# Optimization experiments

Hardware: AMD Instinct MI355X
Metric: run time of the kernel (lower is better)

Reference implementation:

```python
import jax, jax.numpy as jnp
import numpy as np

N_NODES = 50000
N_EDGES = 800000
N_ENTS = 200000
N_RELS = 500
D = 128


def setup_inputs() -> dict:
    key = jax.random.key(0)
    ks = jax.random.split(key, 9)
    return {
        "prev_ent_embs": jax.random.normal(ks[0], (N_ENTS, D), dtype=jnp.float32),
        "rel_embs": jax.random.normal(ks[1], (N_RELS, D), dtype=jnp.float32),
        "loop_weight": jax.random.normal(ks[2], (D, D), dtype=jnp.float32) * 0.1,
        "evolve_loop_weight": jax.random.normal(ks[3], (D, D), dtype=jnp.float32) * 0.1,
        "weight_neighbor": jax.random.normal(ks[4], (D, D), dtype=jnp.float32) * 0.1,
        "node_id": jax.random.randint(ks[5], (N_NODES,), 0, N_ENTS, dtype=jnp.int64) if jax.config.jax_enable_x64 else jax.random.randint(ks[5], (N_NODES,), 0, N_ENTS, dtype=jnp.int32),
        "src": jax.random.randint(ks[6], (N_EDGES,), 0, N_NODES, dtype=jnp.int32),
        "dst": jax.random.randint(ks[7], (N_EDGES,), 0, N_NODES, dtype=jnp.int32),
        "etype": jax.random.randint(ks[8], (N_EDGES,), 0, N_RELS, dtype=jnp.int32),
    }


def reference(prev_ent_embs, rel_embs, loop_weight, evolve_loop_weight,
              weight_neighbor, node_id, src, dst, etype):
    n_nodes = node_id.shape[0]
    # node features gathered from global entity table
    h = prev_ent_embs[node_id]                                    # [N, D]

    # per-edge message: (h[src] + rel[type]) @ W_neighbor
    msg = (h[src] + rel_embs[etype]) @ weight_neighbor            # [E, D]

    # scatter-sum into destination nodes
    agg = jax.ops.segment_sum(msg, dst, num_segments=n_nodes)     # [N, D]

    # in-degree and norm (apply_func: h * in_norm, standard 1/in_degree)
    deg = jax.ops.segment_sum(jnp.ones_like(dst, dtype=h.dtype), dst,
                              num_segments=n_nodes)               # [N]
    has_in = deg > 0
    in_norm = jnp.where(has_in, 1.0 / jnp.maximum(deg, 1.0), 0.0)[:, None]
    agg = agg * in_norm

    # self-loop: loop_weight where in_degree>0, evolve_loop_weight otherwise
    loop_msg = jnp.where(has_in[:, None], h @ loop_weight, h @ evolve_loop_weight)

    # activation (dropout=0 -> identity in eval)
    return jax.nn.relu(agg + loop_msg)
```

## Files before the change

### kernel.cpp

```cpp
#include <hip/hip_runtime.h>
#include <hip/hip_bf16.h>
#include <stdint.h>

#define N_NODES 50000
#define N_EDGES 800000
#define N_ENTS  200000
#define N_RELS  500
#define DIM     128

#define DEGS 16

using f32x4  = __attribute__((ext_vector_type(4))) float;
using bf16x8 = __attribute__((ext_vector_type(8))) short;

static __device__ __forceinline__ ushort f_to_bf16(float f) {
    __hip_bfloat16 h = __float2bfloat16(f);
    return *reinterpret_cast<ushort*>(&h);
}
static __device__ __forceinline__ uint pack2(float a, float b) {
    return (uint)f_to_bf16(a) | ((uint)f_to_bf16(b) << 16);
}
static __device__ __forceinline__ float blo(uint u) { return __uint_as_float(u << 16); }
static __device__ __forceinline__ float bhi(uint u) { return __uint_as_float(u & 0xffff0000u); }

__global__ __launch_bounds__(256) void k_front(
        const float* __restrict__ prev, const int* __restrict__ node_id,
        ushort* __restrict__ afull,
        const int* __restrict__ dst, int* __restrict__ deg,
        ushort* __restrict__ r16,
        const float* __restrict__ rel, ushort* __restrict__ rel_bf,
        const float* __restrict__ Wn, const float* __restrict__ Wl,
        ushort* __restrict__ WfT) {
    int blk = blockIdx.x;
    if (blk < 3125) {
        int e = blk * 256 + threadIdx.x;
        if (e < N_EDGES) {
            int r = atomicAdd(&deg[dst[e] * DEGS], 1);
            r16[e] = (ushort)r;
        }
    } else if (blk < 6250) {
        int i = (blk - 3125) * 256 + threadIdx.x;
        int row = i >> 4, c = (i & 15) * 8;
        int nid = node_id[row];
        const float* p = prev + (size_t)nid * DIM + c;
        float4 v0 = *(const float4*)p;
        float4 v1 = *(const float4*)(p + 4);
        uint4 w;
        w.x = pack2(v0.x, v0.y);
        w.y = pack2(v0.z, v0.w);
        w.z = pack2(v1.x, v1.y);
        w.w = pack2(v1.z, v1.w);
        *(uint4*)(afull + (size_t)row * 256 + 128 + c) = w;
    } else {
        int i = (blk - 6250) * 256 + threadIdx.x;
        if (i < 128 * 256) {
            int n = i >> 8, k = i & 255;
            float v = (k < 128) ? Wn[k * 128 + n] : Wl[(k - 128) * 128 + n];
            WfT[i] = f_to_bf16(v);
        } else {
            int j = i - 128 * 256;
            if (j < N_RELS * 64) {
                float2 v = *(const float2*)(rel + j * 2);
                *(uint*)(rel_bf + j * 2) = pack2(v.x, v.y);
            }
        }
    }
}

__global__ __launch_bounds__(256) void k_offs(const int* __restrict__ deg,
                                              int* __restrict__ counter,
                                              int* __restrict__ offs) {
    int i = blockIdx.x * 256 + threadIdx.x;
    int lane = threadIdx.x & 63;
    int v = (i < N_NODES) ? deg[i * DEGS] : 0;
    int inc = v;
#pragma unroll
    for (int o = 1; o < 64; o <<= 1) {
        int u = __shfl_up(inc, o);
        if (lane >= o) inc += u;
    }
    int wsum = __shfl(inc, 63);
    int base = 0;
    if (lane == 0) base = atomicAdd(counter, wsum);
    base = __shfl(base, 0);
    if (i < N_NODES) offs[i] = base + inc - v;
}

__global__ __launch_bounds__(256) void k_scatter(const int* __restrict__ dst,
                                                 const int* __restrict__ src,
                                                 const int* __restrict__ etype,
                                                 const ushort* __restrict__ r16,
                                                 const int* __restrict__ offs,
                                                 uint* __restrict__ srcpk) {
    int e = blockIdx.x * blockDim.x + threadIdx.x;
    if (e < N_EDGES) {
        uint rec = (uint)src[e] | ((uint)etype[e] << 16);
        int p = offs[dst[e]] + (int)r16[e];
        srcpk[p] = rec;
    }
}

__global__ __launch_bounds__(256) void k_agg(ushort* __restrict__ afull,
                                             const ushort* __restrict__ rel_bf,
                                             const uint* __restrict__ srcpk,
                                             const int* __restrict__ offs,
                                             const int* __restrict__ deg) {
    int wave = threadIdx.x >> 6, lane = threadIdx.x & 63;
    int n = blockIdx.x * 4 + wave;
    if (n >= N_NODES) return;
    int off = offs[n], d = deg[n * DEGS];
    int c = lane * 2;
    const ushort* hb = afull + 128 + c;
    const ushort* rb = rel_bf + c;
    float a0 = 0.f, a1 = 0.f;
    for (int b0 = 0; b0 < d; b0 += 64) {
        int cnt = min(64, d - b0);
        int rec = (lane < cnt) ? (int)srcpk[off + b0 + lane] : 0;
        int j = 0;
        for (; j + 8 <= cnt; j += 8) {
            uint h0, h1, h2, h3, h4, h5, h6, h7;
            uint r0, r1, r2, r3, r4, r5, r6, r7;
            {
                uint e0 = (uint)__shfl(rec, j);
                uint e1 = (uint)__shfl(rec, j + 1);
                uint e2 = (uint)__shfl(rec, j + 2);
                uint e3 = (uint)__shfl(rec, j + 3);
                uint e4 = (uint)__shfl(rec, j + 4);
                uint e5 = (uint)__shfl(rec, j + 5);
                uint e6 = (uint)__shfl(rec, j + 6);
                uint e7 = (uint)__shfl(rec, j + 7);
                h0 = *(const uint*)(hb + (size_t)(e0 & 0xffffu) * 256);
                r0 = *(const uint*)(rb + (e0 >> 16) * 128);
                h1 = *(const uint*)(hb + (size_t)(e1 & 0xffffu) * 256);
                r1 = *(const uint*)(rb + (e1 >> 16) * 128);
                h2 = *(const uint*)(hb + (size_t)(e2 & 0xffffu) * 256);
                r2 = *(const uint*)(rb + (e2 >> 16) * 128);
                h3 = *(const uint*)(hb + (size_t)(e3 & 0xffffu) * 256);
                r3 = *(const uint*)(rb + (e3 >> 16) * 128);
                h4 = *(const uint*)(hb + (size_t)(e4 & 0xffffu) * 256);
                r4 = *(const uint*)(rb + (e4 >> 16) * 128);
                h5 = *(const uint*)(hb + (size_t)(e5 & 0xffffu) * 256);
                r5 = *(const uint*)(rb + (e5 >> 16) * 128);
                h6 = *(const uint*)(hb + (size_t)(e6 & 0xffffu) * 256);
                r6 = *(const uint*)(rb + (e6 >> 16) * 128);
                h7 = *(const uint*)(hb + (size_t)(e7 & 0xffffu) * 256);
                r7 = *(const uint*)(rb + (e7 >> 16) * 128);
            }
            a0 += blo(h0) + blo(r0); a1 += bhi(h0) + bhi(r0);
            a0 += blo(h1) + blo(r1); a1 += bhi(h1) + bhi(r1);
            a0 += blo(h2) + blo(r2); a1 += bhi(h2) + bhi(r2);
            a0 += blo(h3) + blo(r3); a1 += bhi(h3) + bhi(r3);
            a0 += blo(h4) + blo(r4); a1 += bhi(h4) + bhi(r4);
            a0 += blo(h5) + blo(r5); a1 += bhi(h5) + bhi(r5);
            a0 += blo(h6) + blo(r6); a1 += bhi(h6) + bhi(r6);
            a0 += blo(h7) + blo(r7); a1 += bhi(h7) + bhi(r7);
        }
        for (; j < cnt; j++) {
            uint e0 = (uint)__shfl(rec, j);
            uint h0 = *(const uint*)(hb + (size_t)(e0 & 0xffffu) * 256);
            uint r0 = *(const uint*)(rb + (e0 >> 16) * 128);
            a0 += blo(h0) + blo(r0); a1 += bhi(h0) + bhi(r0);
        }
    }
    float norm = (d > 0) ? 1.0f / (float)d : 0.0f;
    *(uint*)(afull + (size_t)n * 256 + c) = pack2(a0 * norm, a1 * norm);
}

#define LDSK 264
__global__ __launch_bounds__(256) void k_mm(const ushort* __restrict__ afull,
                                            const ushort* __restrict__ WfT,
                                            float* __restrict__ out) {
    __shared__ ushort wl[128 * LDSK];
    for (int idx = threadIdx.x; idx < 128 * 32; idx += 256) {
        int n = idx >> 5, p = idx & 31;
        uint4 v = *(const uint4*)(WfT + n * 256 + p * 8);
        *(uint4*)(&wl[n * LDSK + p * 8]) = v;
    }
    __syncthreads();

    int wave = threadIdx.x >> 6, lane = threadIdx.x & 63;
    int m = lane & 15, quad = lane >> 4;
    int rowBase = blockIdx.x * 128 + wave * 32;

    f32x4 acc[2][8];
#pragma unroll
    for (int rt = 0; rt < 2; rt++)
#pragma unroll
        for (int ct = 0; ct < 8; ct++) acc[rt][ct] = f32x4{0.f, 0.f, 0.f, 0.f};

    int r0 = rowBase + m;      if (r0 > N_NODES - 1) r0 = N_NODES - 1;
    int r1 = rowBase + 16 + m; if (r1 > N_NODES - 1) r1 = N_NODES - 1;
    const ushort* pa0 = afull + (size_t)r0 * 256 + quad * 8;
    const ushort* pa1 = afull + (size_t)r1 * 256 + quad * 8;

#pragma unroll
    for (int ks = 0; ks < 8; ks++) {
        bf16x8 a0 = *(const bf16x8*)(pa0 + ks * 32);
        bf16x8 a1 = *(const bf16x8*)(pa1 + ks * 32);
#pragma unroll
        for (int ct = 0; ct < 8; ct++) {
            bf16x8 b = *(const bf16x8*)(&wl[(ct * 16 + m) * LDSK + ks * 32 + quad * 8]);
            acc[0][ct] = __builtin_amdgcn_mfma_f32_16x16x32_bf16(a0, b, acc[0][ct], 0, 0, 0);
            acc[1][ct] = __builtin_amdgcn_mfma_f32_16x16x32_bf16(a1, b, acc[1][ct], 0, 0, 0);
        }
    }

#pragma unroll
    for (int rt = 0; rt < 2; rt++) {
        int rbase = rowBase + rt * 16 + quad * 4;
#pragma unroll
        for (int reg = 0; reg < 4; reg++) {
            int grow = rbase + reg;
            if (grow < N_NODES) {
#pragma unroll
                for (int ct = 0; ct < 8; ct++) {
                    float v = acc[rt][ct][reg];
                    out[(size_t)grow * 128 + ct * 16 + m] = v > 0.f ? v : 0.f;
                }
            }
        }
    }
}

__global__ void k_fixup(const ushort* __restrict__ afull,
                        const float* __restrict__ We,
                        const int* __restrict__ deg,
                        float* __restrict__ out) {
    int wave = threadIdx.x >> 6, lane = threadIdx.x & 63;
    int n = blockIdx.x * 4 + wave;
    if (n >= N_NODES) return;
    if (deg[n * DEGS] != 0) return;
    int c = lane * 2;
    float a0 = 0.f, a1 = 0.f;
    for (int k = 0; k < 128; k++) {
        float h = blo((uint)afull[(size_t)n * 256 + 128 + k]);
        a0 += h * We[k * 128 + c];
        a1 += h * We[k * 128 + c + 1];
    }
    out[(size_t)n * 128 + c]     = a0 > 0.f ? a0 : 0.f;
    out[(size_t)n * 128 + c + 1] = a1 > 0.f ? a1 : 0.f;
}

extern "C" void kernel_launch(void* const* d_in, const int* in_sizes, int n_in,
                              void* d_out, int out_size, void* d_ws, size_t ws_size,
                              hipStream_t stream) {
    const float* prev  = (const float*)d_in[0];
    const float* rel   = (const float*)d_in[1];
    const float* Wl    = (const float*)d_in[2];
    const float* We    = (const float*)d_in[3];
    const float* Wn    = (const float*)d_in[4];
    const int* node_id = (const int*)d_in[5];
    const int* src     = (const int*)d_in[6];
    const int* dst     = (const int*)d_in[7];
    const int* etype   = (const int*)d_in[8];
    float* out = (float*)d_out;

    char* ws = (char*)d_ws;
    ushort* afull  = (ushort*)(ws);
    ushort* WfT    = (ushort*)(ws + 25600000);
    ushort* rel_bf = (ushort*)(ws + 25665536);
    int* deg       = (int*)(ws + 25793536);
    int* counter   = (int*)(ws + 28993536);
    int* offs      = (int*)(ws + 28993600);
    ushort* r16    = (ushort*)(ws + 29193600);
    uint* srcpk    = (uint*)(ws + 30793600);

    hipMemsetAsync(deg, 0, 3200064, stream);
    k_front   <<<6504, 256, 0, stream>>>(prev, node_id, afull, dst, deg, r16,
                                         rel, rel_bf, Wn, Wl, WfT);
    k_offs    <<<196,  256, 0, stream>>>(deg, counter, offs);
    k_scatter <<<3125, 256, 0, stream>>>(dst, src, etype, r16, offs, srcpk);
    k_agg     <<<12500, 256, 0, stream>>>(afull, rel_bf, srcpk, offs, deg);
    k_mm      <<<391,  256, 0, stream>>>(afull, WfT, out);
    k_fixup   <<<12500, 256, 0, stream>>>(afull, We, deg, out);
}
```

Before: 265.2 us.

## Gather neighbor rows with 16-byte loads across four edge groups per wave

The aggregation kernel now splits each wave into four lane groups of 16. Each lane loads 8 bf16 values per edge with uint4 loads, so a wave processes 8 edges per iteration, and the partial sums are combined with cross-lane shuffles. Tail edges point at a zero-filled sentinel node row and relation row, written by an extra front-kernel block, which removes the remainder loop. A compact degree array replaces the strided 16-int-padded degree reads. This trades more accumulator registers and some padded wasted loads for wider, fewer memory transactions.

```diff
diff --git a/kernel.cpp b/kernel.cpp
--- a/kernel.cpp
+++ b/kernel.cpp
@@ -9,6 +9,8 @@
 #define DIM     128
 
 #define DEGS 16
+
+#define ZERO_REC ((int)(50000u | (500u << 16)))
 
 using f32x4  = __attribute__((ext_vector_type(4))) float;
 using bf16x8 = __attribute__((ext_vector_type(8))) short;
@@ -51,7 +53,7 @@
         w.z = pack2(v1.x, v1.y);
         w.w = pack2(v1.z, v1.w);
         *(uint4*)(afull + (size_t)row * 256 + 128 + c) = w;
-    } else {
+    } else if (blk < 6504) {
         int i = (blk - 6250) * 256 + threadIdx.x;
         if (i < 128 * 256) {
             int n = i >> 8, k = i & 255;
@@ -64,12 +66,17 @@
                 *(uint*)(rel_bf + j * 2) = pack2(v.x, v.y);
             }
         }
+    } else {
+        int t = threadIdx.x;
+        if (t < 128)       ((uint*)(afull + (size_t)50000 * 256))[t] = 0u;
+        else if (t < 192)  ((uint*)(rel_bf + 500 * 128))[t - 128]    = 0u;
     }
 }
 
 __global__ __launch_bounds__(256) void k_offs(const int* __restrict__ deg,
                                               int* __restrict__ counter,
-                                              int* __restrict__ offs) {
+                                              int* __restrict__ offs,
+                                              int* __restrict__ degc) {
     int i = blockIdx.x * 256 + threadIdx.x;
     int lane = threadIdx.x & 63;
     int v = (i < N_NODES) ? deg[i * DEGS] : 0;
@@ -83,7 +90,10 @@
     int base = 0;
     if (lane == 0) base = atomicAdd(counter, wsum);
     base = __shfl(base, 0);
-    if (i < N_NODES) offs[i] = base + inc - v;
+    if (i < N_NODES) {
+        offs[i] = base + inc - v;
+        degc[i] = v;
+    }
 }
 
 __global__ __launch_bounds__(256) void k_scatter(const int* __restrict__ dst,
@@ -104,66 +114,52 @@
                                              const ushort* __restrict__ rel_bf,
                                              const uint* __restrict__ srcpk,
                                              const int* __restrict__ offs,
-                                             const int* __restrict__ deg) {
+                                             const int* __restrict__ degc) {
     int wave = threadIdx.x >> 6, lane = threadIdx.x & 63;
     int n = blockIdx.x * 4 + wave;
     if (n >= N_NODES) return;
-    int off = offs[n], d = deg[n * DEGS];
-    int c = lane * 2;
-    const ushort* hb = afull + 128 + c;
-    const ushort* rb = rel_bf + c;
-    float a0 = 0.f, a1 = 0.f;
+    int off = offs[n], d = degc[n];
+    int g = lane >> 4, q = lane & 15;
+    const ushort* hb = afull + 128 + q * 8;
+    const ushort* rb = rel_bf + q * 8;
+    float acc[8] = {0.f, 0.f, 0.f, 0.f, 0.f, 0.f, 0.f, 0.f};
+
+#define ACC4(hv, rv)                                              \
+    acc[0] += blo(hv.x) + blo(rv.x); acc[1] += bhi(hv.x) + bhi(rv.x); \
+    acc[2] += blo(hv.y) + blo(rv.y); acc[3] += bhi(hv.y) + bhi(rv.y); \
+    acc[4] += blo(hv.z) + blo(rv.z); acc[5] += bhi(hv.z) + bhi(rv.z); \
+    acc[6] += blo(hv.w) + blo(rv.w); acc[7] += bhi(hv.w) + bhi(rv.w);
+
     for (int b0 = 0; b0 < d; b0 += 64) {
         int cnt = min(64, d - b0);
-        int rec = (lane < cnt) ? (int)srcpk[off + b0 + lane] : 0;
-        int j = 0;
-        for (; j + 8 <= cnt; j += 8) {
-            uint h0, h1, h2, h3, h4, h5, h6, h7;
-            uint r0, r1, r2, r3, r4, r5, r6, r7;
-            {
-                uint e0 = (uint)__shfl(rec, j);
-                uint e1 = (uint)__shfl(rec, j + 1);
-                uint e2 = (uint)__shfl(rec, j + 2);
-                uint e3 = (uint)__shfl(rec, j + 3);
-                uint e4 = (uint)__shfl(rec, j + 4);
-                uint e5 = (uint)__shfl(rec, j + 5);
-                uint e6 = (uint)__shfl(rec, j + 6);
-                uint e7 = (uint)__shfl(rec, j + 7);
-                h0 = *(const uint*)(hb + (size_t)(e0 & 0xffffu) * 256);
-                r0 = *(const uint*)(rb + (e0 >> 16) * 128);
-                h1 = *(const uint*)(hb + (size_t)(e1 & 0xffffu) * 256);
-                r1 = *(const uint*)(rb + (e1 >> 16) * 128);
-                h2 = *(const uint*)(hb + (size_t)(e2 & 0xffffu) * 256);
-                r2 = *(const uint*)(rb + (e2 >> 16) * 128);
-                h3 = *(const uint*)(hb + (size_t)(e3 & 0xffffu) * 256);
-                r3 = *(const uint*)(rb + (e3 >> 16) * 128);
-                h4 = *(const uint*)(hb + (size_t)(e4 & 0xffffu) * 256);
-                r4 = *(const uint*)(rb + (e4 >> 16) * 128);
-                h5 = *(const uint*)(hb + (size_t)(e5 & 0xffffu) * 256);
-                r5 = *(const uint*)(rb + (e5 >> 16) * 128);
-                h6 = *(const uint*)(hb + (size_t)(e6 & 0xffffu) * 256);
-                r6 = *(const uint*)(rb + (e6 >> 16) * 128);
-                h7 = *(const uint*)(hb + (size_t)(e7 & 0xffffu) * 256);
-                r7 = *(const uint*)(rb + (e7 >> 16) * 128);
-            }
-            a0 += blo(h0) + blo(r0); a1 += bhi(h0) + bhi(r0);
-            a0 += blo(h1) + blo(r1); a1 += bhi(h1) + bhi(r1);
-            a0 += blo(h2) + blo(r2); a1 += bhi(h2) + bhi(r2);
-            a0 += blo(h3) + blo(r3); a1 += bhi(h3) + bhi(r3);
-            a0 += blo(h4) + blo(r4); a1 += bhi(h4) + bhi(r4);
-            a0 += blo(h5) + blo(r5); a1 += bhi(h5) + bhi(r5);
-            a0 += blo(h6) + blo(r6); a1 += bhi(h6) + bhi(r6);
-            a0 += blo(h7) + blo(r7); a1 += bhi(h7) + bhi(r7);
-        }
-        for (; j < cnt; j++) {
-            uint e0 = (uint)__shfl(rec, j);
-            uint h0 = *(const uint*)(hb + (size_t)(e0 & 0xffffu) * 256);
-            uint r0 = *(const uint*)(rb + (e0 >> 16) * 128);
-            a0 += blo(h0) + blo(r0); a1 += bhi(h0) + bhi(r0);
-        }
+        int rec = (lane < cnt) ? (int)srcpk[off + b0 + lane] : ZERO_REC;
+        for (int j = 0; j < cnt; j += 8) {
+            uint e0 = (uint)__shfl(rec, j + g);
+            uint e1 = (uint)__shfl(rec, j + 4 + g);
+            uint4 h0 = *(const uint4*)(hb + (size_t)(e0 & 0xffffu) * 256);
+            uint4 r0 = *(const uint4*)(rb + (e0 >> 16) * 128);
+            uint4 h1 = *(const uint4*)(hb + (size_t)(e1 & 0xffffu) * 256);
+            uint4 r1 = *(const uint4*)(rb + (e1 >> 16) * 128);
+            ACC4(h0, r0);
+            ACC4(h1, r1);
+        }
+    }
+#undef ACC4
+
+#pragma unroll
+    for (int i = 0; i < 8; i++) {
+        acc[i] += __shfl_xor(acc[i], 16);
+        acc[i] += __shfl_xor(acc[i], 32);
     }
     float norm = (d > 0) ? 1.0f / (float)d : 0.0f;
-    *(uint*)(afull + (size_t)n * 256 + c) = pack2(a0 * norm, a1 * norm);
+    if (g == 0) {
+        uint4 w;
+        w.x = pack2(acc[0] * norm, acc[1] * norm);
+        w.y = pack2(acc[2] * norm, acc[3] * norm);
+        w.z = pack2(acc[4] * norm, acc[5] * norm);
+        w.w = pack2(acc[6] * norm, acc[7] * norm);
+        *(uint4*)(afull + (size_t)n * 256 + q * 8) = w;
+    }
 }
 
 #define LDSK 264
@@ -224,12 +220,12 @@
 
 __global__ void k_fixup(const ushort* __restrict__ afull,
                         const float* __restrict__ We,
-                        const int* __restrict__ deg,
+                        const int* __restrict__ degc,
                         float* __restrict__ out) {
     int wave = threadIdx.x >> 6, lane = threadIdx.x & 63;
     int n = blockIdx.x * 4 + wave;
     if (n >= N_NODES) return;
-    if (deg[n * DEGS] != 0) return;
+    if (degc[n] != 0) return;
     int c = lane * 2;
     float a0 = 0.f, a1 = 0.f;
     for (int k = 0; k < 128; k++) {
@@ -257,20 +253,21 @@
 
     char* ws = (char*)d_ws;
     ushort* afull  = (ushort*)(ws);
-    ushort* WfT    = (ushort*)(ws + 25600000);
-    ushort* rel_bf = (ushort*)(ws + 25665536);
-    int* deg       = (int*)(ws + 25793536);
-    int* counter   = (int*)(ws + 28993536);
-    int* offs      = (int*)(ws + 28993600);
-    ushort* r16    = (ushort*)(ws + 29193600);
-    uint* srcpk    = (uint*)(ws + 30793600);
+    ushort* WfT    = (ushort*)(ws + 25600512);
+    ushort* rel_bf = (ushort*)(ws + 25666048);
+    int* deg       = (int*)(ws + 25794304);
+    int* counter   = (int*)(ws + 28994304);
+    int* offs      = (int*)(ws + 28994368);
+    int* degc      = (int*)(ws + 29194368);
+    ushort* r16    = (ushort*)(ws + 29394368);
+    uint* srcpk    = (uint*)(ws + 30994368);
 
     hipMemsetAsync(deg, 0, 3200064, stream);
-    k_front   <<<6504, 256, 0, stream>>>(prev, node_id, afull, dst, deg, r16,
+    k_front   <<<6505, 256, 0, stream>>>(prev, node_id, afull, dst, deg, r16,
                                          rel, rel_bf, Wn, Wl, WfT);
-    k_offs    <<<196,  256, 0, stream>>>(deg, counter, offs);
+    k_offs    <<<196,  256, 0, stream>>>(deg, counter, offs, degc);
     k_scatter <<<3125, 256, 0, stream>>>(dst, src, etype, r16, offs, srcpk);
-    k_agg     <<<12500, 256, 0, stream>>>(afull, rel_bf, srcpk, offs, deg);
+    k_agg     <<<12500, 256, 0, stream>>>(afull, rel_bf, srcpk, offs, degc);
     k_mm      <<<391,  256, 0, stream>>>(afull, WfT, out);
-    k_fixup   <<<12500, 256, 0, stream>>>(afull, We, deg, out);
-}
+    k_fixup   <<<12500, 256, 0, stream>>>(afull, We, degc, out);
+}
```

New measurement: 264.3 us. Within noise of the previous version (-0.3%).
